# Optimization experiments

Measured on AMD Instinct MI355X. Metric: run time of the kernel, lower is better.

## Reference

```python
import jax, jax.numpy as jnp
import numpy as np

DN = ('NCHW', 'OIHW', 'NCHW')

def setup_inputs() -> dict:
    key = jax.random.key(0)
    ks = jax.random.split(key, 7)
    N, C_in, H, W = 32, 512, 56, 56
    C_sq, C_e1, C_e3 = 64, 256, 256
    def p(k, shape, fan_in):
        bound = 1.0 / np.sqrt(fan_in)
        return jax.random.uniform(k, shape, jnp.float32, -bound, bound)
    return {
        'x': jax.random.normal(ks[0], (N, C_in, H, W), jnp.float32),
        'w_sq': p(ks[1], (C_sq, C_in, 1, 1), C_in),
        'b_sq': p(ks[2], (C_sq,), C_in),
        'w_1x1': p(ks[3], (C_e1, C_sq, 1, 1), C_sq),
        'b_1x1': p(ks[4], (C_e1,), C_sq),
        'w_3x3': p(ks[5], (C_e3, C_sq, 3, 3), C_sq * 9),
        'b_3x3': p(ks[6], (C_e3,), C_sq * 9),
    }

def reference(x, w_sq, b_sq, w_1x1, b_1x1, w_3x3, b_3x3):
    # squeeze: 1x1 conv + ReLU
    s = jax.lax.conv_general_dilated(x, w_sq, (1, 1), 'VALID', dimension_numbers=DN)
    s = jax.nn.relu(s + b_sq[None, :, None, None])
    # expand 1x1 branch
    e1 = jax.lax.conv_general_dilated(s, w_1x1, (1, 1), 'VALID', dimension_numbers=DN)
    e1 = jax.nn.relu(e1 + b_1x1[None, :, None, None])
    # expand 3x3 branch, padding=1
    e3 = jax.lax.conv_general_dilated(s, w_3x3, (1, 1), ((1, 1), (1, 1)), dimension_numbers=DN)
    e3 = jax.nn.relu(e3 + b_3x3[None, :, None, None])
    return jnp.concatenate([e1, e3], axis=1)
```

## Files before the change

kernel.cpp:

```cpp
#include <hip/hip_runtime.h>
#include <hip/hip_bf16.h>
#include <stdint.h>

typedef __attribute__((ext_vector_type(8))) short bf16x8;
typedef __attribute__((ext_vector_type(4))) float f32x4;

#define GLB(p) ((const __attribute__((address_space(1))) void*)(p))
#define LDSP(p) ((__attribute__((address_space(3))) void*)(p))

#define HW    3136
#define WIMG  56
#define PROW  58
#define PNR   59
#define SIMG  (PNR * PROW)
#define C_IN  512

static __device__ __forceinline__ unsigned short f2bf(float f) {
    unsigned u = __builtin_bit_cast(unsigned, f);
    return (unsigned short)((u + 0x7FFFu + ((u >> 16) & 1u)) >> 16);
}

__global__ void prep_kernel(const float* __restrict__ wsq,
                            const float* __restrict__ w1,
                            const float* __restrict__ w3,
                            unsigned short* __restrict__ wsq_bf,
                            unsigned short* __restrict__ w1_bf,
                            unsigned short* __restrict__ w3r_bf,
                            unsigned short* __restrict__ s) {
    const int b = blockIdx.x, tid = threadIdx.x;
    if (b < 576) {
        int t = b * 256 + tid;
        if (t < 32768) wsq_bf[t] = f2bf(wsq[t]);
        if (t < 16384) w1_bf[t] = f2bf(w1[t]);
        int j = t >> 14, rem = t & 16383;
        int o = rem >> 6, c = rem & 63;
        w3r_bf[t] = f2bf(w3[(o * 64 + c) * 9 + j]);
    } else {
        const int img = b - 576;
        uint4* sn = (uint4*)(s + (size_t)img * SIMG * 64);
        uint4 z; z.x = z.y = z.z = z.w = 0;
        for (int t = tid; t < 1824; t += 256) {
            int cell = t >> 3, q = t & 7;
            int row, col;
            if (cell < 116) { row = (cell >= 58) ? 57 : 0; col = cell % 58; }
            else { int c2 = cell - 116; row = 1 + (c2 >> 1); col = (c2 & 1) * 57; }
            sn[(size_t)(row * PROW + col) * 8 + q] = z;
        }
    }
}

__global__ __launch_bounds__(256, 4) void squeeze_kernel(
    const float* __restrict__ x, const float* __restrict__ b_sq,
    const unsigned short* __restrict__ wsq_bf, unsigned short* __restrict__ s)
{
    __shared__ uint8_t xs[2][8192];
    const int n = blockIdx.y, hw0 = blockIdx.x * 64;
    const int tid = threadIdx.x;
    const int w = tid >> 6, l = tid & 63, lx = l & 15, lk = l >> 4;

    const uint8_t* xbase = (const uint8_t*)(x + (size_t)n * C_IN * HW + hw0);

    auto stage = [&](int buf, int kb) {
        #pragma unroll
        for (int q = 0; q < 2; ++q) {
            int c = q * 256 + tid;
            int r = c >> 4, g = c & 15;
            const uint8_t* src = xbase + (size_t)(kb * 32 + r) * (HW * 4)
                                       + ((g * 16) ^ (((r >> 3) & 3) << 6));
            __builtin_amdgcn_global_load_lds(GLB(src), LDSP(&xs[buf][c * 16]), 16, 0, 0);
        }
    };

    stage(0, 0);
    __syncthreads();

    f32x4 acc[4] = {};
    const unsigned short* ap = wsq_bf + lx * C_IN + lk * 8;
    const int colb4 = ((w * 16 + lx) * 4);
    const int swz = lk << 6;

    for (int kb = 0; kb < 16; ++kb) {
        const int cur = kb & 1;
        if (kb < 15) stage(cur ^ 1, kb + 1);
        const uint8_t* bbase = &xs[cur][lk * 2048 + (colb4 ^ swz)];
        float f[8];
        #pragma unroll
        for (int i = 0; i < 8; ++i) f[i] = *(const float*)(bbase + i * 256);
        union { uint32_t u[4]; bf16x8 v; } bb;
        #pragma unroll
        for (int h = 0; h < 4; ++h)
            asm("v_cvt_pk_bf16_f32 %0, %1, %2" : "=v"(bb.u[h]) : "v"(f[2*h]), "v"(f[2*h+1]));
        bf16x8 a[4];
        #pragma unroll
        for (int mt = 0; mt < 4; ++mt)
            a[mt] = *(const bf16x8*)(ap + mt * 16 * C_IN + kb * 32);
        #pragma unroll
        for (int mt = 0; mt < 4; ++mt)
            acc[mt] = __builtin_amdgcn_mfma_f32_16x16x32_bf16(a[mt], bb.v, acc[mt], 0, 0, 0);
        __syncthreads();
    }

    const int col = hw0 + w * 16 + lx;
    const int p = col + 59 + 2 * (col / WIMG);
    uint8_t* sn = (uint8_t*)s + (size_t)n * SIMG * 128 + (size_t)p * 128;
    const int psw = (p & 7) << 4;
    #pragma unroll
    for (int mt = 0; mt < 4; ++mt) {
        const int c0 = mt * 16 + lk * 4;
        float4 bias = *(const float4*)(b_sq + c0);
        const float* bp = (const float*)&bias;
        unsigned short v[4];
        #pragma unroll
        for (int r = 0; r < 4; ++r) v[r] = f2bf(fmaxf(acc[mt][r] + bp[r], 0.0f));
        uint2 pk;
        pk.x = (unsigned)v[0] | ((unsigned)v[1] << 16);
        pk.y = (unsigned)v[2] | ((unsigned)v[3] << 16);
        *(uint2*)(sn + ((c0 * 2) ^ psw)) = pk;
    }
}

__global__ __launch_bounds__(256, 4) void expand_kernel(
    const unsigned short* __restrict__ s,
    const unsigned short* __restrict__ w1_bf,
    const unsigned short* __restrict__ w3r_bf,
    const float* __restrict__ b1, const float* __restrict__ b3,
    float* __restrict__ out)
{
    __shared__ uint8_t tile[37120];
    const int bid = blockIdx.x;
    const int ord = (bid & 7) * 784 + (bid >> 3);
    const int n = ord / 196;
    const int r2 = ord - n * 196;
    const int mt = r2 / 49;
    const int ht = r2 - mt * 49;
    const int hw0 = ht * 64, y0 = hw0 / WIMG;

    const int tid = threadIdx.x;
    const int w = tid >> 6, l = tid & 63, lx = l & 15, lk = l >> 4;
    const int wm = w >> 1, wn = w & 1;

    const uint8_t* src = (const uint8_t*)s + ((size_t)n * SIMG + y0 * PROW) * 128;
    #pragma unroll
    for (int it = 0; it < 9; ++it) {
        int c = it * 256 + tid;
        __builtin_amdgcn_global_load_lds(GLB(src + (size_t)c * 16), LDSP(&tile[c * 16]), 16, 0, 0);
    }
    if (tid < 16)
        __builtin_amdgcn_global_load_lds(GLB(src + (size_t)(2304 + tid) * 16),
                                         LDSP(&tile[(2304 + tid) * 16]), 16, 0, 0);
    __syncthreads();

    const int cb = mt * 64 + wm * 32;
    const int hb = hw0 + wn * 32;
    int pg[2], tb[2];
    #pragma unroll
    for (int nf = 0; nf < 2; ++nf) {
        int hw = hb + nf * 16 + lx;
        int p = hw + 59 + 2 * (hw / WIMG);
        pg[nf] = p;
        tb[nf] = (p - y0 * PROW) * 128;
    }
    const int lk16 = lk * 16;
    float* outn = out + (size_t)n * 512 * HW;

    {
        f32x4 acc[2][2] = {};
        #pragma unroll
        for (int k0 = 0; k0 < 2; ++k0) {
            bf16x8 bw[2], av[2];
            #pragma unroll
            for (int bt = 0; bt < 2; ++bt)
                bw[bt] = *(const bf16x8*)(w1_bf + (cb + bt * 16 + lx) * 64 + k0 * 32 + lk * 8);
            #pragma unroll
            for (int nf = 0; nf < 2; ++nf)
                av[nf] = *(const bf16x8*)&tile[tb[nf] + ((lk16 + k0 * 64) ^ ((pg[nf] & 7) << 4))];
            #pragma unroll
            for (int bt = 0; bt < 2; ++bt)
                #pragma unroll
                for (int nf = 0; nf < 2; ++nf)
                    acc[bt][nf] = __builtin_amdgcn_mfma_f32_16x16x32_bf16(av[nf], bw[bt], acc[bt][nf], 0, 0, 0);
        }
        #pragma unroll
        for (int bt = 0; bt < 2; ++bt) {
            float bias = b1[cb + bt * 16 + lx];
            float* op = outn + (size_t)(cb + bt * 16 + lx) * HW + hb + lk * 4;
            #pragma unroll
            for (int nf = 0; nf < 2; ++nf) {
                float4 v;
                v.x = fmaxf(acc[bt][nf][0] + bias, 0.0f);
                v.y = fmaxf(acc[bt][nf][1] + bias, 0.0f);
                v.z = fmaxf(acc[bt][nf][2] + bias, 0.0f);
                v.w = fmaxf(acc[bt][nf][3] + bias, 0.0f);
                *(float4*)(op + nf * 16) = v;
            }
        }
    }

    {
        f32x4 acc[2][2] = {};
        #pragma unroll
        for (int j = 0; j < 9; ++j) {
            const int doff = (j / 3 - 1) * PROW + (j % 3 - 1);
            const unsigned short* wj = w3r_bf + j * 16384;
            #pragma unroll
            for (int k0 = 0; k0 < 2; ++k0) {
                bf16x8 bw[2], av[2];
                #pragma unroll
                for (int bt = 0; bt < 2; ++bt)
                    bw[bt] = *(const bf16x8*)(wj + (cb + bt * 16 + lx) * 64 + k0 * 32 + lk * 8);
                #pragma unroll
                for (int nf = 0; nf < 2; ++nf) {
                    int pt = pg[nf] + doff;
                    av[nf] = *(const bf16x8*)&tile[tb[nf] + doff * 128 +
                                                  ((lk16 + k0 * 64) ^ ((pt & 7) << 4))];
                }
                #pragma unroll
                for (int bt = 0; bt < 2; ++bt)
                    #pragma unroll
                    for (int nf = 0; nf < 2; ++nf)
                        acc[bt][nf] = __builtin_amdgcn_mfma_f32_16x16x32_bf16(av[nf], bw[bt], acc[bt][nf], 0, 0, 0);
            }
        }
        #pragma unroll
        for (int bt = 0; bt < 2; ++bt) {
            float bias = b3[cb + bt * 16 + lx];
            float* op = outn + (size_t)(256 + cb + bt * 16 + lx) * HW + hb + lk * 4;
            #pragma unroll
            for (int nf = 0; nf < 2; ++nf) {
                float4 v;
                v.x = fmaxf(acc[bt][nf][0] + bias, 0.0f);
                v.y = fmaxf(acc[bt][nf][1] + bias, 0.0f);
                v.z = fmaxf(acc[bt][nf][2] + bias, 0.0f);
                v.w = fmaxf(acc[bt][nf][3] + bias, 0.0f);
                *(float4*)(op + nf * 16) = v;
            }
        }
    }
}

extern "C" void kernel_launch(void* const* d_in, const int* in_sizes, int n_in,
                              void* d_out, int out_size, void* d_ws, size_t ws_size,
                              hipStream_t stream) {
    const float* x   = (const float*)d_in[0];
    const float* wsq = (const float*)d_in[1];
    const float* bsq = (const float*)d_in[2];
    const float* w1  = (const float*)d_in[3];
    const float* b1  = (const float*)d_in[4];
    const float* w3  = (const float*)d_in[5];
    const float* b3  = (const float*)d_in[6];
    float* out = (float*)d_out;

    unsigned short* wsq_bf = (unsigned short*)d_ws;
    unsigned short* w1_bf  = wsq_bf + 32768;
    unsigned short* w3r_bf = w1_bf + 16384;
    unsigned short* s      = w3r_bf + 147456;

    prep_kernel<<<608, 256, 0, stream>>>(wsq, w1, w3, wsq_bf, w1_bf, w3r_bf, s);
    squeeze_kernel<<<dim3(49, 32), 256, 0, stream>>>(x, bsq, wsq_bf, s);
    expand_kernel<<<6272, 256, 0, stream>>>(s, w1_bf, w3r_bf, b1, b3, out);
}
```

Baseline: 467.8 us.

## Make expand kernel persistent with register-held weights and prefetched tiles; drop squeeze LDS staging

The expand kernel now runs 896 blocks of 512 threads. Each block handles 7 consecutive spatial tiles, keeps its 3x3 and 1x1 weight fragments in registers for all of them, and prefetches the next input tile into registers while computing the current one. Each wave now covers 16 output channels instead of 32. The squeeze kernel drops its double-buffered LDS staging and reads x directly from global memory, with no barriers. This trades more register pressure and uncoalesced-looking strided global reads in squeeze for fewer weight reloads and launch overhead in expand.

```diff
diff --git a/kernel.cpp b/kernel.cpp
--- a/kernel.cpp
+++ b/kernel.cpp
@@ -53,39 +53,20 @@
     const float* __restrict__ x, const float* __restrict__ b_sq,
     const unsigned short* __restrict__ wsq_bf, unsigned short* __restrict__ s)
 {
-    __shared__ uint8_t xs[2][8192];
     const int n = blockIdx.y, hw0 = blockIdx.x * 64;
     const int tid = threadIdx.x;
     const int w = tid >> 6, l = tid & 63, lx = l & 15, lk = l >> 4;
-
-    const uint8_t* xbase = (const uint8_t*)(x + (size_t)n * C_IN * HW + hw0);
-
-    auto stage = [&](int buf, int kb) {
-        #pragma unroll
-        for (int q = 0; q < 2; ++q) {
-            int c = q * 256 + tid;
-            int r = c >> 4, g = c & 15;
-            const uint8_t* src = xbase + (size_t)(kb * 32 + r) * (HW * 4)
-                                       + ((g * 16) ^ (((r >> 3) & 3) << 6));
-            __builtin_amdgcn_global_load_lds(GLB(src), LDSP(&xs[buf][c * 16]), 16, 0, 0);
-        }
-    };
-
-    stage(0, 0);
-    __syncthreads();
+    const int col = hw0 + w * 16 + lx;
+
+    const float* xp = x + (size_t)n * C_IN * HW + col;
+    const unsigned short* ap = wsq_bf + lx * C_IN + lk * 8;
 
     f32x4 acc[4] = {};
-    const unsigned short* ap = wsq_bf + lx * C_IN + lk * 8;
-    const int colb4 = ((w * 16 + lx) * 4);
-    const int swz = lk << 6;
-
     for (int kb = 0; kb < 16; ++kb) {
-        const int cur = kb & 1;
-        if (kb < 15) stage(cur ^ 1, kb + 1);
-        const uint8_t* bbase = &xs[cur][lk * 2048 + (colb4 ^ swz)];
+        const int kbase = kb * 32 + lk * 8;
         float f[8];
         #pragma unroll
-        for (int i = 0; i < 8; ++i) f[i] = *(const float*)(bbase + i * 256);
+        for (int i = 0; i < 8; ++i) f[i] = xp[(size_t)(kbase + i) * HW];
         union { uint32_t u[4]; bf16x8 v; } bb;
         #pragma unroll
         for (int h = 0; h < 4; ++h)
@@ -97,10 +78,8 @@
         #pragma unroll
         for (int mt = 0; mt < 4; ++mt)
             acc[mt] = __builtin_amdgcn_mfma_f32_16x16x32_bf16(a[mt], bb.v, acc[mt], 0, 0, 0);
-        __syncthreads();
-    }
-
-    const int col = hw0 + w * 16 + lx;
+    }
+
     const int p = col + 59 + 2 * (col / WIMG);
     uint8_t* sn = (uint8_t*)s + (size_t)n * SIMG * 128 + (size_t)p * 128;
     const int psw = (p & 7) << 4;
@@ -119,7 +98,7 @@
     }
 }
 
-__global__ __launch_bounds__(256, 4) void expand_kernel(
+__global__ __launch_bounds__(512, 2) void expand_kernel(
     const unsigned short* __restrict__ s,
     const unsigned short* __restrict__ w1_bf,
     const unsigned short* __restrict__ w3r_bf,
@@ -128,110 +107,125 @@
 {
     __shared__ uint8_t tile[37120];
     const int bid = blockIdx.x;
-    const int ord = (bid & 7) * 784 + (bid >> 3);
-    const int n = ord / 196;
-    const int r2 = ord - n * 196;
-    const int mt = r2 / 49;
-    const int ht = r2 - mt * 49;
-    const int hw0 = ht * 64, y0 = hw0 / WIMG;
+    const int ord = (bid & 7) * 112 + (bid >> 3);
+    const int n  = ord / 28;
+    const int r2 = ord - n * 28;
+    const int mt = r2 / 7;
+    const int tg = r2 - mt * 7;
 
     const int tid = threadIdx.x;
     const int w = tid >> 6, l = tid & 63, lx = l & 15, lk = l >> 4;
     const int wm = w >> 1, wn = w & 1;
-
-    const uint8_t* src = (const uint8_t*)s + ((size_t)n * SIMG + y0 * PROW) * 128;
+    const int cb = mt * 64 + wm * 16;
+    const int lk16 = lk * 16;
+
+    bf16x8 w1f[2], w3f[9][2];
     #pragma unroll
-    for (int it = 0; it < 9; ++it) {
-        int c = it * 256 + tid;
-        __builtin_amdgcn_global_load_lds(GLB(src + (size_t)c * 16), LDSP(&tile[c * 16]), 16, 0, 0);
-    }
-    if (tid < 16)
-        __builtin_amdgcn_global_load_lds(GLB(src + (size_t)(2304 + tid) * 16),
-                                         LDSP(&tile[(2304 + tid) * 16]), 16, 0, 0);
-    __syncthreads();
-
-    const int cb = mt * 64 + wm * 32;
-    const int hb = hw0 + wn * 32;
-    int pg[2], tb[2];
+    for (int k0 = 0; k0 < 2; ++k0)
+        w1f[k0] = *(const bf16x8*)(w1_bf + (cb + lx) * 64 + k0 * 32 + lk * 8);
     #pragma unroll
-    for (int nf = 0; nf < 2; ++nf) {
-        int hw = hb + nf * 16 + lx;
-        int p = hw + 59 + 2 * (hw / WIMG);
-        pg[nf] = p;
-        tb[nf] = (p - y0 * PROW) * 128;
-    }
-    const int lk16 = lk * 16;
+    for (int j = 0; j < 9; ++j)
+        #pragma unroll
+        for (int k0 = 0; k0 < 2; ++k0)
+            w3f[j][k0] = *(const bf16x8*)(w3r_bf + j * 16384 + (cb + lx) * 64 + k0 * 32 + lk * 8);
+
+    const float bias1 = b1[cb + lx];
+    const float bias3 = b3[cb + lx];
+    const uint8_t* sn = (const uint8_t*)s + (size_t)n * SIMG * 128;
     float* outn = out + (size_t)n * 512 * HW;
 
+    uint4 g[5];
     {
-        f32x4 acc[2][2] = {};
-        #pragma unroll
-        for (int k0 = 0; k0 < 2; ++k0) {
-            bf16x8 bw[2], av[2];
-            #pragma unroll
-            for (int bt = 0; bt < 2; ++bt)
-                bw[bt] = *(const bf16x8*)(w1_bf + (cb + bt * 16 + lx) * 64 + k0 * 32 + lk * 8);
-            #pragma unroll
-            for (int nf = 0; nf < 2; ++nf)
-                av[nf] = *(const bf16x8*)&tile[tb[nf] + ((lk16 + k0 * 64) ^ ((pg[nf] & 7) << 4))];
-            #pragma unroll
-            for (int bt = 0; bt < 2; ++bt)
+        const int y0 = (tg * 7 * 64) / WIMG;
+        const uint8_t* src = sn + (size_t)y0 * PROW * 128;
+        #pragma unroll
+        for (int it = 0; it < 4; ++it)
+            g[it] = *(const uint4*)(src + (size_t)(it * 512 + tid) * 16);
+        if (tid < 272) g[4] = *(const uint4*)(src + (size_t)(2048 + tid) * 16);
+    }
+
+    for (int t = 0; t < 7; ++t) {
+        const int ht  = tg * 7 + t;
+        const int hw0 = ht * 64;
+        const int cy0 = hw0 / WIMG;
+
+        __syncthreads();
+        #pragma unroll
+        for (int it = 0; it < 4; ++it)
+            *(uint4*)&tile[(it * 512 + tid) * 16] = g[it];
+        if (tid < 272) *(uint4*)&tile[(2048 + tid) * 16] = g[4];
+        __syncthreads();
+
+        if (t < 6) {
+            const int ny0 = ((ht + 1) * 64) / WIMG;
+            const uint8_t* src = sn + (size_t)ny0 * PROW * 128;
+            #pragma unroll
+            for (int it = 0; it < 4; ++it)
+                g[it] = *(const uint4*)(src + (size_t)(it * 512 + tid) * 16);
+            if (tid < 272) g[4] = *(const uint4*)(src + (size_t)(2048 + tid) * 16);
+        }
+
+        const int hb = hw0 + wn * 32;
+        int pg[2], tb[2];
+        #pragma unroll
+        for (int nf = 0; nf < 2; ++nf) {
+            int hw = hb + nf * 16 + lx;
+            int p = hw + 59 + 2 * (hw / WIMG);
+            pg[nf] = p;
+            tb[nf] = (p - cy0 * PROW) * 128;
+        }
+
+        {
+            f32x4 acc[2] = {};
+            #pragma unroll
+            for (int k0 = 0; k0 < 2; ++k0) {
+                bf16x8 av[2];
                 #pragma unroll
                 for (int nf = 0; nf < 2; ++nf)
-                    acc[bt][nf] = __builtin_amdgcn_mfma_f32_16x16x32_bf16(av[nf], bw[bt], acc[bt][nf], 0, 0, 0);
-        }
-        #pragma unroll
-        for (int bt = 0; bt < 2; ++bt) {
-            float bias = b1[cb + bt * 16 + lx];
-            float* op = outn + (size_t)(cb + bt * 16 + lx) * HW + hb + lk * 4;
+                    av[nf] = *(const bf16x8*)&tile[tb[nf] + ((lk16 + k0 * 64) ^ ((pg[nf] & 7) << 4))];
+                #pragma unroll
+                for (int nf = 0; nf < 2; ++nf)
+                    acc[nf] = __builtin_amdgcn_mfma_f32_16x16x32_bf16(av[nf], w1f[k0], acc[nf], 0, 0, 0);
+            }
+            float* op = outn + (size_t)(cb + lx) * HW + hb + lk * 4;
             #pragma unroll
             for (int nf = 0; nf < 2; ++nf) {
                 float4 v;
-                v.x = fmaxf(acc[bt][nf][0] + bias, 0.0f);
-                v.y = fmaxf(acc[bt][nf][1] + bias, 0.0f);
-                v.z = fmaxf(acc[bt][nf][2] + bias, 0.0f);
-                v.w = fmaxf(acc[bt][nf][3] + bias, 0.0f);
+                v.x = fmaxf(acc[nf][0] + bias1, 0.0f);
+                v.y = fmaxf(acc[nf][1] + bias1, 0.0f);
+                v.z = fmaxf(acc[nf][2] + bias1, 0.0f);
+                v.w = fmaxf(acc[nf][3] + bias1, 0.0f);
                 *(float4*)(op + nf * 16) = v;
             }
         }
-    }
-
-    {
-        f32x4 acc[2][2] = {};
-        #pragma unroll
-        for (int j = 0; j < 9; ++j) {
-            const int doff = (j / 3 - 1) * PROW + (j % 3 - 1);
-            const unsigned short* wj = w3r_bf + j * 16384;
-            #pragma unroll
-            for (int k0 = 0; k0 < 2; ++k0) {
-                bf16x8 bw[2], av[2];
+
+        {
+            f32x4 acc[2] = {};
+            #pragma unroll
+            for (int j = 0; j < 9; ++j) {
+                const int doff = (j / 3 - 1) * PROW + (j % 3 - 1);
                 #pragma unroll
-                for (int bt = 0; bt < 2; ++bt)
-                    bw[bt] = *(const bf16x8*)(wj + (cb + bt * 16 + lx) * 64 + k0 * 32 + lk * 8);
-                #pragma unroll
-                for (int nf = 0; nf < 2; ++nf) {
-                    int pt = pg[nf] + doff;
-                    av[nf] = *(const bf16x8*)&tile[tb[nf] + doff * 128 +
-                                                  ((lk16 + k0 * 64) ^ ((pt & 7) << 4))];
-                }
-                #pragma unroll
-                for (int bt = 0; bt < 2; ++bt)
+                for (int k0 = 0; k0 < 2; ++k0) {
+                    bf16x8 av[2];
+                    #pragma unroll
+                    for (int nf = 0; nf < 2; ++nf) {
+                        int pt = pg[nf] + doff;
+                        av[nf] = *(const bf16x8*)&tile[tb[nf] + doff * 128 +
+                                                      ((lk16 + k0 * 64) ^ ((pt & 7) << 4))];
+                    }
                     #pragma unroll
                     for (int nf = 0; nf < 2; ++nf)
-                        acc[bt][nf] = __builtin_amdgcn_mfma_f32_16x16x32_bf16(av[nf], bw[bt], acc[bt][nf], 0, 0, 0);
-            }
-        }
-        #pragma unroll
-        for (int bt = 0; bt < 2; ++bt) {
-            float bias = b3[cb + bt * 16 + lx];
-            float* op = outn + (size_t)(256 + cb + bt * 16 + lx) * HW + hb + lk * 4;
+                        acc[nf] = __builtin_amdgcn_mfma_f32_16x16x32_bf16(av[nf], w3f[j][k0], acc[nf], 0, 0, 0);
+                }
+            }
+            float* op = outn + (size_t)(256 + cb + lx) * HW + hb + lk * 4;
             #pragma unroll
             for (int nf = 0; nf < 2; ++nf) {
                 float4 v;
-                v.x = fmaxf(acc[bt][nf][0] + bias, 0.0f);
-                v.y = fmaxf(acc[bt][nf][1] + bias, 0.0f);
-                v.z = fmaxf(acc[bt][nf][2] + bias, 0.0f);
-                v.w = fmaxf(acc[bt][nf][3] + bias, 0.0f);
+                v.x = fmaxf(acc[nf][0] + bias3, 0.0f);
+                v.y = fmaxf(acc[nf][1] + bias3, 0.0f);
+                v.z = fmaxf(acc[nf][2] + bias3, 0.0f);
+                v.w = fmaxf(acc[nf][3] + bias3, 0.0f);
                 *(float4*)(op + nf * 16) = v;
             }
         }
@@ -257,5 +251,5 @@
 
     prep_kernel<<<608, 256, 0, stream>>>(wsq, w1, w3, wsq_bf, w1_bf, w3r_bf, s);
     squeeze_kernel<<<dim3(49, 32), 256, 0, stream>>>(x, bsq, wsq_bf, s);
-    expand_kernel<<<6272, 256, 0, stream>>>(s, w1_bf, w3r_bf, b1, b3, out);
-}
+    expand_kernel<<<896, 512, 0, stream>>>(s, w1_bf, w3r_bf, b1, b3, out);
+}
```

Result: slower. 485.1 us (+3.7%).
